# Optimization experiments

Measured on AMD Instinct MI355X. Metric: run time of the kernel, lower is better.

Reference implementation:

```python
import jax, jax.numpy as jnp
import numpy as np

N_ITEMS = 100000
N_USERS = 16384
HIST = 50
TEXT_DIM = 256
GCN_DIM = 128
HIDDEN_DIM = 512
TOWER_DIM = 128


def _l2norm(x, eps=1e-12):
    # F.normalize(dim=1): x / max(||x||, eps)
    n = jnp.sqrt(jnp.sum(x * x, axis=1, keepdims=True))
    return x / jnp.maximum(n, eps)


def setup_inputs() -> dict:
    key = jax.random.key(0)
    ks = jax.random.split(key, 10)
    s1i = 1.0 / np.sqrt(TEXT_DIM + GCN_DIM)
    s2i = 1.0 / np.sqrt(HIDDEN_DIM)
    s1u = 1.0 / np.sqrt(GCN_DIM + TOWER_DIM)
    return {
        "item_text_emb": jax.random.normal(ks[0], (N_ITEMS, TEXT_DIM), jnp.float32),
        "gcn_item_emb": jax.random.normal(ks[1], (N_ITEMS, GCN_DIM), jnp.float32),
        "gcn_user_emb": jax.random.normal(ks[2], (N_USERS, GCN_DIM), jnp.float32),
        "hist_idx": jax.random.randint(ks[3], (N_USERS, HIST), 0, N_ITEMS),
        "W1i": jax.random.normal(ks[4], (TEXT_DIM + GCN_DIM, HIDDEN_DIM), jnp.float32) * s1i,
        "b1i": jnp.zeros((HIDDEN_DIM,), jnp.float32),
        "W2i": jax.random.normal(ks[5], (HIDDEN_DIM, TOWER_DIM), jnp.float32) * s2i,
        "b2i": jnp.zeros((TOWER_DIM,), jnp.float32),
        "W1u": jax.random.normal(ks[6], (GCN_DIM + TOWER_DIM, HIDDEN_DIM), jnp.float32) * s1u,
        "b1u": jnp.zeros((HIDDEN_DIM,), jnp.float32),
        "W2u": jax.random.normal(ks[7], (HIDDEN_DIM, TOWER_DIM), jnp.float32) * s2i,
        "b2u": jnp.zeros((TOWER_DIM,), jnp.float32),
    }


def reference(item_text_emb, gcn_item_emb, gcn_user_emb, hist_idx,
              W1i, b1i, W2i, b2i, W1u, b1u, W2u, b2u):
    # encode_items: MLP over concat(text, gcn) features, then L2 normalize
    item_feat = jnp.concatenate([item_text_emb, gcn_item_emb], axis=1)  # [N_items, text+gcn]
    h = jax.nn.relu(item_feat @ W1i + b1i)
    item_emb = _l2norm(h @ W2i + b2i)  # [N_items, TOWER_DIM]
    # encode_users: per-user gather of history item embeddings + mean pooling
    hist = jnp.mean(item_emb[hist_idx], axis=1)  # [N_users, TOWER_DIM]
    fused = jnp.concatenate([gcn_user_emb, hist], axis=1)
    hu = jax.nn.relu(fused @ W1u + b1u)
    user_emb = _l2norm(hu @ W2u + b2u)  # [N_users, TOWER_DIM]
    return user_emb
```

## Files before the change

### kernel.cpp

```cpp
#include <hip/hip_runtime.h>
#include <hip/hip_bf16.h>

#define HIST 50

typedef __bf16 bf8 __attribute__((ext_vector_type(8)));
typedef float  f4  __attribute__((ext_vector_type(4)));

__device__ __forceinline__ unsigned short f2bf(float x) {
    unsigned u = __builtin_bit_cast(unsigned, x);
    u += 0x7fffu + ((u >> 16) & 1u);
    return (unsigned short)(u >> 16);
}
__device__ __forceinline__ float bf2f(unsigned b) {
    unsigned u = b << 16;
    return __builtin_bit_cast(float, u);
}

__global__ void pack_weights(const float* __restrict__ W1i, const float* __restrict__ W2i,
                             const float* __restrict__ W1u, const float* __restrict__ W2u,
                             unsigned short* __restrict__ dstbase)
{
    int i = blockIdx.x * 256 + threadIdx.x;
    const float* W; unsigned short* dst; int N, KS, loc;
    if (i < 24576)      { W = W1i; dst = dstbase;          N = 512; KS = 12; loc = i; }
    else if (i < 32768) { W = W2i; dst = dstbase + 196608; N = 128; KS = 16; loc = i - 24576; }
    else if (i < 49152) { W = W1u; dst = dstbase + 262144; N = 512; KS = 8;  loc = i - 32768; }
    else                { W = W2u; dst = dstbase + 393216; N = 128; KS = 16; loc = i - 49152; }
    int l = loc & 63, fi = loc >> 6;
    int ks = fi % KS, nt = fi / KS;
    int q = l >> 4, c = l & 15;
    const float* src = W + (size_t)(ks * 32 + q * 8) * N + nt * 16 + c;
    unsigned o[4];
    #pragma unroll
    for (int k = 0; k < 4; ++k) {
        unsigned lo = f2bf(src[(2 * k) * N]);
        unsigned hi = f2bf(src[(2 * k + 1) * N]);
        o[k] = lo | (hi << 16);
    }
    uint4 v; v.x = o[0]; v.y = o[1]; v.z = o[2]; v.w = o[3];
    ((uint4*)dst)[(size_t)(nt * KS + ks) * 64 + l] = v;
}

template<int KS1, int ASTR, bool OUT_BF16>
__device__ __forceinline__ void two_layer(
    const unsigned short* As, unsigned short* Hs,
    const float* b1s, const float* b2s, float* sumsq,
    const bf8* __restrict__ w1f, const bf8* __restrict__ w2f,
    void* __restrict__ outp, int row0, int tid)
{
    const int HSTR = 528;
    const int l = tid & 63, w = tid >> 6;
    const int q = l >> 4, c = l & 15;

    f4 acc1[2][8];
    #pragma unroll
    for (int i = 0; i < 2; ++i)
        #pragma unroll
        for (int j = 0; j < 8; ++j) acc1[i][j] = (f4)0.0f;

    const unsigned short* a0p = As + c * ASTR + q * 8;
    const unsigned short* a1p = As + (16 + c) * ASTR + q * 8;
    for (int ks = 0; ks < KS1; ++ks) {
        bf8 a0 = *(const bf8*)(a0p + ks * 32);
        bf8 a1 = *(const bf8*)(a1p + ks * 32);
        const bf8* wp = w1f + ((size_t)(w * 8) * KS1 + ks) * 64 + l;
        #pragma unroll
        for (int nt = 0; nt < 8; ++nt) {
            bf8 b = wp[(size_t)nt * KS1 * 64];
            acc1[0][nt] = __builtin_amdgcn_mfma_f32_16x16x32_bf16(a0, b, acc1[0][nt], 0, 0, 0);
            acc1[1][nt] = __builtin_amdgcn_mfma_f32_16x16x32_bf16(a1, b, acc1[1][nt], 0, 0, 0);
        }
    }
    #pragma unroll
    for (int nt = 0; nt < 8; ++nt) {
        int col = (w * 8 + nt) * 16 + c;
        float bias = b1s[col];
        #pragma unroll
        for (int rt = 0; rt < 2; ++rt)
            #pragma unroll
            for (int reg = 0; reg < 4; ++reg) {
                float h = fmaxf(acc1[rt][nt][reg] + bias, 0.0f);
                Hs[(rt * 16 + q * 4 + reg) * HSTR + col] = f2bf(h);
            }
    }
    __syncthreads();

    f4 acc2[2][2];
    #pragma unroll
    for (int i = 0; i < 2; ++i)
        #pragma unroll
        for (int j = 0; j < 2; ++j) acc2[i][j] = (f4)0.0f;

    const unsigned short* h0p = Hs + c * HSTR + q * 8;
    const unsigned short* h1p = Hs + (16 + c) * HSTR + q * 8;
    for (int ks = 0; ks < 16; ++ks) {
        bf8 a0 = *(const bf8*)(h0p + ks * 32);
        bf8 a1 = *(const bf8*)(h1p + ks * 32);
        #pragma unroll
        for (int j = 0; j < 2; ++j) {
            bf8 b = w2f[(size_t)((w * 2 + j) * 16 + ks) * 64 + l];
            acc2[0][j] = __builtin_amdgcn_mfma_f32_16x16x32_bf16(a0, b, acc2[0][j], 0, 0, 0);
            acc2[1][j] = __builtin_amdgcn_mfma_f32_16x16x32_bf16(a1, b, acc2[1][j], 0, 0, 0);
        }
    }
    float v[2][2][4];
    #pragma unroll
    for (int rt = 0; rt < 2; ++rt)
        #pragma unroll
        for (int j = 0; j < 2; ++j)
            #pragma unroll
            for (int reg = 0; reg < 4; ++reg)
                v[rt][j][reg] = acc2[rt][j][reg] + b2s[(w * 2 + j) * 16 + c];
    #pragma unroll
    for (int rt = 0; rt < 2; ++rt)
        #pragma unroll
        for (int reg = 0; reg < 4; ++reg) {
            float s = v[rt][0][reg] * v[rt][0][reg] + v[rt][1][reg] * v[rt][1][reg];
            s += __shfl_xor(s, 1); s += __shfl_xor(s, 2);
            s += __shfl_xor(s, 4); s += __shfl_xor(s, 8);
            if (c == 0) atomicAdd(&sumsq[rt * 16 + q * 4 + reg], s);
        }
    __syncthreads();
    #pragma unroll
    for (int rt = 0; rt < 2; ++rt)
        #pragma unroll
        for (int reg = 0; reg < 4; ++reg) {
            int row = rt * 16 + q * 4 + reg;
            float inv = 1.0f / fmaxf(sqrtf(sumsq[row]), 1e-12f);
            #pragma unroll
            for (int j = 0; j < 2; ++j) {
                int col = (w * 2 + j) * 16 + c;
                float o = v[rt][j][reg] * inv;
                if (OUT_BF16)
                    ((unsigned short*)outp)[(size_t)(row0 + row) * 128 + col] = f2bf(o);
                else
                    ((float*)outp)[(size_t)(row0 + row) * 128 + col] = o;
            }
        }
}

__global__ __launch_bounds__(256, 2) void item_kernel(
    const float* __restrict__ text, const float* __restrict__ gcn,
    const bf8* __restrict__ w1f, const float* __restrict__ b1,
    const bf8* __restrict__ w2f, const float* __restrict__ b2,
    unsigned short* __restrict__ item_bf)
{
    __shared__ unsigned short As[32 * 392];
    __shared__ unsigned short Hs[32 * 528];
    __shared__ float b1s[512], b2s[128], sumsq[32];
    const int tid = threadIdx.x;
    const int row0 = blockIdx.x * 32;
    const float4* t4 = (const float4*)text;
    const float4* g4 = (const float4*)gcn;
    #pragma unroll
    for (int j = 0; j < 8; ++j) {
        int idx = tid + j * 256; int r = idx >> 6, c4 = idx & 63;
        float4 x = t4[(size_t)(row0 + r) * 64 + c4];
        ushort4 s; s.x = f2bf(x.x); s.y = f2bf(x.y); s.z = f2bf(x.z); s.w = f2bf(x.w);
        *(ushort4*)(As + r * 392 + c4 * 4) = s;
    }
    #pragma unroll
    for (int j = 0; j < 4; ++j) {
        int idx = tid + j * 256; int r = idx >> 5, c4 = idx & 31;
        float4 x = g4[(size_t)(row0 + r) * 32 + c4];
        ushort4 s; s.x = f2bf(x.x); s.y = f2bf(x.y); s.z = f2bf(x.z); s.w = f2bf(x.w);
        *(ushort4*)(As + r * 392 + 256 + c4 * 4) = s;
    }
    b1s[tid] = b1[tid]; b1s[tid + 256] = b1[tid + 256];
    if (tid < 128) b2s[tid] = b2[tid];
    if (tid < 32)  sumsq[tid] = 0.0f;
    __syncthreads();
    two_layer<12, 392, true>(As, Hs, b1s, b2s, sumsq, w1f, w2f, item_bf, row0, tid);
}

__global__ __launch_bounds__(256, 2) void user_kernel(
    const float* __restrict__ gcnu, const int* __restrict__ hist,
    const unsigned short* __restrict__ item_bf,
    const bf8* __restrict__ w1f, const float* __restrict__ b1,
    const bf8* __restrict__ w2f, const float* __restrict__ b2,
    float* __restrict__ outp)
{
    __shared__ unsigned short As[32 * 272];
    __shared__ unsigned short Hs[32 * 528];
    __shared__ float b1s[512], b2s[128], sumsq[32];
    const int tid = threadIdx.x;
    const int u0 = blockIdx.x * 32;
    const float4* g4 = (const float4*)gcnu;
    #pragma unroll
    for (int j = 0; j < 4; ++j) {
        int idx = tid + j * 256; int r = idx >> 5, c4 = idx & 31;
        float4 x = g4[(size_t)(u0 + r) * 32 + c4];
        ushort4 s; s.x = f2bf(x.x); s.y = f2bf(x.y); s.z = f2bf(x.z); s.w = f2bf(x.w);
        *(ushort4*)(As + r * 272 + c4 * 4) = s;
    }
    {
        const int u = tid >> 3, g = tid & 7;
        float f[16];
        #pragma unroll
        for (int k = 0; k < 16; ++k) f[k] = 0.0f;
        const int* hrow = hist + (size_t)(u0 + u) * HIST;
        #pragma unroll 4
        for (int t = 0; t < HIST; ++t) {
            int id = hrow[t];
            const uint4* p = (const uint4*)(item_bf + (size_t)id * 128 + g * 16);
            uint4 x0 = p[0], x1 = p[1];
            unsigned vs[8] = {x0.x, x0.y, x0.z, x0.w, x1.x, x1.y, x1.z, x1.w};
            #pragma unroll
            for (int k = 0; k < 8; ++k) {
                f[2 * k]     += bf2f(vs[k] & 0xffffu);
                f[2 * k + 1] += bf2f(vs[k] >> 16);
            }
        }
        unsigned o[8];
        #pragma unroll
        for (int k = 0; k < 8; ++k)
            o[k] = (unsigned)f2bf(f[2 * k] * 0.02f) | ((unsigned)f2bf(f[2 * k + 1] * 0.02f) << 16);
        uint4 s0; s0.x = o[0]; s0.y = o[1]; s0.z = o[2]; s0.w = o[3];
        uint4 s1; s1.x = o[4]; s1.y = o[5]; s1.z = o[6]; s1.w = o[7];
        *(uint4*)(As + u * 272 + 128 + g * 16) = s0;
        *(uint4*)(As + u * 272 + 128 + g * 16 + 8) = s1;
    }
    b1s[tid] = b1[tid]; b1s[tid + 256] = b1[tid + 256];
    if (tid < 128) b2s[tid] = b2[tid];
    if (tid < 32)  sumsq[tid] = 0.0f;
    __syncthreads();
    two_layer<8, 272, false>(As, Hs, b1s, b2s, sumsq, w1f, w2f, outp, u0, tid);
}

extern "C" void kernel_launch(void* const* d_in, const int* in_sizes, int n_in,
                              void* d_out, int out_size, void* d_ws, size_t ws_size,
                              hipStream_t stream) {
    const float* text = (const float*)d_in[0];
    const float* gcni = (const float*)d_in[1];
    const float* gcnu = (const float*)d_in[2];
    const int*   hist = (const int*)d_in[3];
    const float* W1i  = (const float*)d_in[4];
    const float* b1i  = (const float*)d_in[5];
    const float* W2i  = (const float*)d_in[6];
    const float* b2i  = (const float*)d_in[7];
    const float* W1u  = (const float*)d_in[8];
    const float* b1u  = (const float*)d_in[9];
    const float* W2u  = (const float*)d_in[10];
    const float* b2u  = (const float*)d_in[11];
    float* out = (float*)d_out;

    unsigned short* itemb = (unsigned short*)d_ws;
    unsigned short* pw = itemb + 12800000;

    pack_weights<<<224, 256, 0, stream>>>(W1i, W2i, W1u, W2u, pw);
    item_kernel<<<100000 / 32, 256, 0, stream>>>(
        text, gcni, (const bf8*)pw, b1i, (const bf8*)(pw + 196608), b2i, itemb);
    user_kernel<<<16384 / 32, 256, 0, stream>>>(
        gcnu, hist, itemb, (const bf8*)(pw + 262144), b1u, (const bf8*)(pw + 393216), b2u, out);
}
```

Measured before the change: 349.4 us.

## Alias input and hidden LDS tiles, raise occupancy, stage history indices in LDS

The input tile and hidden-activation tile now share one LDS buffer, with a barrier added before the hidden layer overwrites the inputs. The hidden stride is reduced, launch bounds go from 2 to 4 blocks per SM to raise occupancy, and the K loops are fully unrolled. In the user kernel, history indices are bulk-loaded into LDS before the gather, and bias loads move ahead of it. Higher occupancy may force register spills given the 64 accumulator floats per thread, and the extra barrier adds some sync cost.

```diff
diff --git a/kernel.cpp b/kernel.cpp
--- a/kernel.cpp
+++ b/kernel.cpp
@@ -43,12 +43,12 @@
 
 template<int KS1, int ASTR, bool OUT_BF16>
 __device__ __forceinline__ void two_layer(
-    const unsigned short* As, unsigned short* Hs,
+    unsigned short* U,
     const float* b1s, const float* b2s, float* sumsq,
     const bf8* __restrict__ w1f, const bf8* __restrict__ w2f,
     void* __restrict__ outp, int row0, int tid)
 {
-    const int HSTR = 528;
+    const int HSTR = 520;
     const int l = tid & 63, w = tid >> 6;
     const int q = l >> 4, c = l & 15;
 
@@ -58,19 +58,22 @@
         #pragma unroll
         for (int j = 0; j < 8; ++j) acc1[i][j] = (f4)0.0f;
 
-    const unsigned short* a0p = As + c * ASTR + q * 8;
-    const unsigned short* a1p = As + (16 + c) * ASTR + q * 8;
+    const unsigned short* a0p = U + c * ASTR + q * 8;
+    const unsigned short* a1p = U + (16 + c) * ASTR + q * 8;
+    const bf8* wp = w1f + (size_t)(w * 8) * KS1 * 64 + l;
+    #pragma unroll
     for (int ks = 0; ks < KS1; ++ks) {
         bf8 a0 = *(const bf8*)(a0p + ks * 32);
         bf8 a1 = *(const bf8*)(a1p + ks * 32);
-        const bf8* wp = w1f + ((size_t)(w * 8) * KS1 + ks) * 64 + l;
         #pragma unroll
         for (int nt = 0; nt < 8; ++nt) {
-            bf8 b = wp[(size_t)nt * KS1 * 64];
+            bf8 b = wp[(size_t)nt * KS1 * 64 + ks * 64];
             acc1[0][nt] = __builtin_amdgcn_mfma_f32_16x16x32_bf16(a0, b, acc1[0][nt], 0, 0, 0);
             acc1[1][nt] = __builtin_amdgcn_mfma_f32_16x16x32_bf16(a1, b, acc1[1][nt], 0, 0, 0);
         }
     }
+    __syncthreads();
+    unsigned short* Hs = U;
     #pragma unroll
     for (int nt = 0; nt < 8; ++nt) {
         int col = (w * 8 + nt) * 16 + c;
@@ -93,6 +96,7 @@
 
     const unsigned short* h0p = Hs + c * HSTR + q * 8;
     const unsigned short* h1p = Hs + (16 + c) * HSTR + q * 8;
+    #pragma unroll
     for (int ks = 0; ks < 16; ++ks) {
         bf8 a0 = *(const bf8*)(h0p + ks * 32);
         bf8 a1 = *(const bf8*)(h1p + ks * 32);
@@ -139,14 +143,13 @@
         }
 }
 
-__global__ __launch_bounds__(256, 2) void item_kernel(
+__global__ __launch_bounds__(256, 4) void item_kernel(
     const float* __restrict__ text, const float* __restrict__ gcn,
     const bf8* __restrict__ w1f, const float* __restrict__ b1,
     const bf8* __restrict__ w2f, const float* __restrict__ b2,
     unsigned short* __restrict__ item_bf)
 {
-    __shared__ unsigned short As[32 * 392];
-    __shared__ unsigned short Hs[32 * 528];
+    __shared__ __align__(16) unsigned short U[32 * 520];
     __shared__ float b1s[512], b2s[128], sumsq[32];
     const int tid = threadIdx.x;
     const int row0 = blockIdx.x * 32;
@@ -157,49 +160,55 @@
         int idx = tid + j * 256; int r = idx >> 6, c4 = idx & 63;
         float4 x = t4[(size_t)(row0 + r) * 64 + c4];
         ushort4 s; s.x = f2bf(x.x); s.y = f2bf(x.y); s.z = f2bf(x.z); s.w = f2bf(x.w);
-        *(ushort4*)(As + r * 392 + c4 * 4) = s;
+        *(ushort4*)(U + r * 392 + c4 * 4) = s;
     }
     #pragma unroll
     for (int j = 0; j < 4; ++j) {
         int idx = tid + j * 256; int r = idx >> 5, c4 = idx & 31;
         float4 x = g4[(size_t)(row0 + r) * 32 + c4];
         ushort4 s; s.x = f2bf(x.x); s.y = f2bf(x.y); s.z = f2bf(x.z); s.w = f2bf(x.w);
-        *(ushort4*)(As + r * 392 + 256 + c4 * 4) = s;
+        *(ushort4*)(U + r * 392 + 256 + c4 * 4) = s;
     }
     b1s[tid] = b1[tid]; b1s[tid + 256] = b1[tid + 256];
     if (tid < 128) b2s[tid] = b2[tid];
     if (tid < 32)  sumsq[tid] = 0.0f;
     __syncthreads();
-    two_layer<12, 392, true>(As, Hs, b1s, b2s, sumsq, w1f, w2f, item_bf, row0, tid);
-}
-
-__global__ __launch_bounds__(256, 2) void user_kernel(
+    two_layer<12, 392, true>(U, b1s, b2s, sumsq, w1f, w2f, item_bf, row0, tid);
+}
+
+__global__ __launch_bounds__(256, 4) void user_kernel(
     const float* __restrict__ gcnu, const int* __restrict__ hist,
     const unsigned short* __restrict__ item_bf,
     const bf8* __restrict__ w1f, const float* __restrict__ b1,
     const bf8* __restrict__ w2f, const float* __restrict__ b2,
     float* __restrict__ outp)
 {
-    __shared__ unsigned short As[32 * 272];
-    __shared__ unsigned short Hs[32 * 528];
+    __shared__ __align__(16) unsigned short U[32 * 520];
     __shared__ float b1s[512], b2s[128], sumsq[32];
     const int tid = threadIdx.x;
     const int u0 = blockIdx.x * 32;
+    int* histL = (int*)(U + 32 * 272);
     const float4* g4 = (const float4*)gcnu;
     #pragma unroll
     for (int j = 0; j < 4; ++j) {
         int idx = tid + j * 256; int r = idx >> 5, c4 = idx & 31;
         float4 x = g4[(size_t)(u0 + r) * 32 + c4];
         ushort4 s; s.x = f2bf(x.x); s.y = f2bf(x.y); s.z = f2bf(x.z); s.w = f2bf(x.w);
-        *(ushort4*)(As + r * 272 + c4 * 4) = s;
-    }
+        *(ushort4*)(U + r * 272 + c4 * 4) = s;
+    }
+    for (int i = tid; i < 32 * HIST; i += 256)
+        histL[i] = hist[(size_t)u0 * HIST + i];
+    b1s[tid] = b1[tid]; b1s[tid + 256] = b1[tid + 256];
+    if (tid < 128) b2s[tid] = b2[tid];
+    if (tid < 32)  sumsq[tid] = 0.0f;
+    __syncthreads();
     {
         const int u = tid >> 3, g = tid & 7;
         float f[16];
         #pragma unroll
         for (int k = 0; k < 16; ++k) f[k] = 0.0f;
-        const int* hrow = hist + (size_t)(u0 + u) * HIST;
-        #pragma unroll 4
+        const int* hrow = histL + u * HIST;
+        #pragma unroll 5
         for (int t = 0; t < HIST; ++t) {
             int id = hrow[t];
             const uint4* p = (const uint4*)(item_bf + (size_t)id * 128 + g * 16);
@@ -217,14 +226,11 @@
             o[k] = (unsigned)f2bf(f[2 * k] * 0.02f) | ((unsigned)f2bf(f[2 * k + 1] * 0.02f) << 16);
         uint4 s0; s0.x = o[0]; s0.y = o[1]; s0.z = o[2]; s0.w = o[3];
         uint4 s1; s1.x = o[4]; s1.y = o[5]; s1.z = o[6]; s1.w = o[7];
-        *(uint4*)(As + u * 272 + 128 + g * 16) = s0;
-        *(uint4*)(As + u * 272 + 128 + g * 16 + 8) = s1;
-    }
-    b1s[tid] = b1[tid]; b1s[tid + 256] = b1[tid + 256];
-    if (tid < 128) b2s[tid] = b2[tid];
-    if (tid < 32)  sumsq[tid] = 0.0f;
-    __syncthreads();
-    two_layer<8, 272, false>(As, Hs, b1s, b2s, sumsq, w1f, w2f, outp, u0, tid);
+        *(uint4*)(U + u * 272 + 128 + g * 16) = s0;
+        *(uint4*)(U + u * 272 + 128 + g * 16 + 8) = s1;
+    }
+    __syncthreads();
+    two_layer<8, 272, false>(U, b1s, b2s, sumsq, w1f, w2f, outp, u0, tid);
 }
 
 extern "C" void kernel_launch(void* const* d_in, const int* in_sizes, int n_in,
```

Result: slower. 366.9 us (+5.0%).

## Double row tile to 64 per block and alias input and hidden LDS buffers

Applied to the files above, without the earlier changes.

Each block now handles 64 rows instead of 32, so every weight fragment fetched from global memory feeds four MFMA row tiles instead of two, halving weight traffic per row. The input and hidden activations now share one LDS buffer, with an extra barrier before the hidden layer overwrites the inputs, which keeps shared memory within budget. The K loops are fully unrolled with all A and B fragments loaded up front, and a tail guard handles the partial last item block. The history gather uses four threads per user instead of eight. The trade-off is higher register pressure from 32 accumulators per thread, which may cut occupancy or cause spills, and fewer blocks to spread across the GPU.

```diff
diff --git a/kernel.cpp b/kernel.cpp
--- a/kernel.cpp
+++ b/kernel.cpp
@@ -2,6 +2,8 @@
 #include <hip/hip_bf16.h>
 
 #define HIST 50
+#define N_ITEMS 100000
+#define N_USERS 16384
 
 typedef __bf16 bf8 __attribute__((ext_vector_type(8)));
 typedef float  f4  __attribute__((ext_vector_type(4)));
@@ -42,77 +44,88 @@
 }
 
 template<int KS1, int ASTR, bool OUT_BF16>
-__device__ __forceinline__ void two_layer(
-    const unsigned short* As, unsigned short* Hs,
-    const float* b1s, const float* b2s, float* sumsq,
+__device__ __forceinline__ void tower_core(
+    unsigned short* U, const float* b1s, const float* b2s, float* sumsq,
     const bf8* __restrict__ w1f, const bf8* __restrict__ w2f,
-    void* __restrict__ outp, int row0, int tid)
-{
-    const int HSTR = 528;
+    void* __restrict__ outp, int row0, int nval, int tid)
+{
+    const int HSTR = 520;
     const int l = tid & 63, w = tid >> 6;
     const int q = l >> 4, c = l & 15;
 
-    f4 acc1[2][8];
-    #pragma unroll
-    for (int i = 0; i < 2; ++i)
+    f4 acc1[4][8];
+    #pragma unroll
+    for (int i = 0; i < 4; ++i)
         #pragma unroll
         for (int j = 0; j < 8; ++j) acc1[i][j] = (f4)0.0f;
 
-    const unsigned short* a0p = As + c * ASTR + q * 8;
-    const unsigned short* a1p = As + (16 + c) * ASTR + q * 8;
+    const unsigned short* ap = U + c * ASTR + q * 8;
+    #pragma unroll
     for (int ks = 0; ks < KS1; ++ks) {
-        bf8 a0 = *(const bf8*)(a0p + ks * 32);
-        bf8 a1 = *(const bf8*)(a1p + ks * 32);
-        const bf8* wp = w1f + ((size_t)(w * 8) * KS1 + ks) * 64 + l;
-        #pragma unroll
-        for (int nt = 0; nt < 8; ++nt) {
-            bf8 b = wp[(size_t)nt * KS1 * 64];
-            acc1[0][nt] = __builtin_amdgcn_mfma_f32_16x16x32_bf16(a0, b, acc1[0][nt], 0, 0, 0);
-            acc1[1][nt] = __builtin_amdgcn_mfma_f32_16x16x32_bf16(a1, b, acc1[1][nt], 0, 0, 0);
-        }
-    }
+        bf8 a[4], b[8];
+        #pragma unroll
+        for (int rt = 0; rt < 4; ++rt)
+            a[rt] = *(const bf8*)(ap + rt * 16 * ASTR + ks * 32);
+        #pragma unroll
+        for (int nt = 0; nt < 8; ++nt)
+            b[nt] = w1f[(size_t)((w * 8 + nt) * KS1 + ks) * 64 + l];
+        #pragma unroll
+        for (int rt = 0; rt < 4; ++rt)
+            #pragma unroll
+            for (int nt = 0; nt < 8; ++nt)
+                acc1[rt][nt] = __builtin_amdgcn_mfma_f32_16x16x32_bf16(a[rt], b[nt], acc1[rt][nt], 0, 0, 0);
+    }
+    __syncthreads();
+
     #pragma unroll
     for (int nt = 0; nt < 8; ++nt) {
-        int col = (w * 8 + nt) * 16 + c;
+        int col = w * 128 + nt * 16 + c;
         float bias = b1s[col];
         #pragma unroll
-        for (int rt = 0; rt < 2; ++rt)
+        for (int rt = 0; rt < 4; ++rt)
             #pragma unroll
             for (int reg = 0; reg < 4; ++reg) {
                 float h = fmaxf(acc1[rt][nt][reg] + bias, 0.0f);
-                Hs[(rt * 16 + q * 4 + reg) * HSTR + col] = f2bf(h);
+                U[(rt * 16 + q * 4 + reg) * HSTR + col] = f2bf(h);
             }
     }
     __syncthreads();
 
-    f4 acc2[2][2];
-    #pragma unroll
-    for (int i = 0; i < 2; ++i)
+    f4 acc2[4][2];
+    #pragma unroll
+    for (int i = 0; i < 4; ++i)
         #pragma unroll
         for (int j = 0; j < 2; ++j) acc2[i][j] = (f4)0.0f;
 
-    const unsigned short* h0p = Hs + c * HSTR + q * 8;
-    const unsigned short* h1p = Hs + (16 + c) * HSTR + q * 8;
+    const unsigned short* hp = U + c * HSTR + q * 8;
+    #pragma unroll
     for (int ks = 0; ks < 16; ++ks) {
-        bf8 a0 = *(const bf8*)(h0p + ks * 32);
-        bf8 a1 = *(const bf8*)(h1p + ks * 32);
+        bf8 a[4], b[2];
+        #pragma unroll
+        for (int rt = 0; rt < 4; ++rt)
+            a[rt] = *(const bf8*)(hp + rt * 16 * HSTR + ks * 32);
+        #pragma unroll
+        for (int j = 0; j < 2; ++j)
+            b[j] = w2f[(size_t)((w * 2 + j) * 16 + ks) * 64 + l];
+        #pragma unroll
+        for (int rt = 0; rt < 4; ++rt)
+            #pragma unroll
+            for (int j = 0; j < 2; ++j)
+                acc2[rt][j] = __builtin_amdgcn_mfma_f32_16x16x32_bf16(a[rt], b[j], acc2[rt][j], 0, 0, 0);
+    }
+
+    float v[4][2][4];
+    #pragma unroll
+    for (int rt = 0; rt < 4; ++rt)
         #pragma unroll
         for (int j = 0; j < 2; ++j) {
-            bf8 b = w2f[(size_t)((w * 2 + j) * 16 + ks) * 64 + l];
-            acc2[0][j] = __builtin_amdgcn_mfma_f32_16x16x32_bf16(a0, b, acc2[0][j], 0, 0, 0);
-            acc2[1][j] = __builtin_amdgcn_mfma_f32_16x16x32_bf16(a1, b, acc2[1][j], 0, 0, 0);
-        }
-    }
-    float v[2][2][4];
-    #pragma unroll
-    for (int rt = 0; rt < 2; ++rt)
-        #pragma unroll
-        for (int j = 0; j < 2; ++j)
+            float bias = b2s[w * 32 + j * 16 + c];
             #pragma unroll
             for (int reg = 0; reg < 4; ++reg)
-                v[rt][j][reg] = acc2[rt][j][reg] + b2s[(w * 2 + j) * 16 + c];
-    #pragma unroll
-    for (int rt = 0; rt < 2; ++rt)
+                v[rt][j][reg] = acc2[rt][j][reg] + bias;
+        }
+    #pragma unroll
+    for (int rt = 0; rt < 4; ++rt)
         #pragma unroll
         for (int reg = 0; reg < 4; ++reg) {
             float s = v[rt][0][reg] * v[rt][0][reg] + v[rt][1][reg] * v[rt][1][reg];
@@ -122,22 +135,27 @@
         }
     __syncthreads();
     #pragma unroll
-    for (int rt = 0; rt < 2; ++rt)
+    for (int rt = 0; rt < 4; ++rt)
         #pragma unroll
         for (int reg = 0; reg < 4; ++reg) {
             int row = rt * 16 + q * 4 + reg;
-            float inv = 1.0f / fmaxf(sqrtf(sumsq[row]), 1e-12f);
-            #pragma unroll
-            for (int j = 0; j < 2; ++j) {
-                int col = (w * 2 + j) * 16 + c;
-                float o = v[rt][j][reg] * inv;
-                if (OUT_BF16)
-                    ((unsigned short*)outp)[(size_t)(row0 + row) * 128 + col] = f2bf(o);
-                else
-                    ((float*)outp)[(size_t)(row0 + row) * 128 + col] = o;
+            if (row < nval) {
+                float inv = 1.0f / fmaxf(sqrtf(sumsq[row]), 1e-12f);
+                #pragma unroll
+                for (int j = 0; j < 2; ++j) {
+                    int col = w * 32 + j * 16 + c;
+                    float o = v[rt][j][reg] * inv;
+                    if (OUT_BF16)
+                        ((unsigned short*)outp)[(size_t)(row0 + row) * 128 + col] = f2bf(o);
+                    else
+                        ((float*)outp)[(size_t)(row0 + row) * 128 + col] = o;
+                }
             }
         }
 }
+
+#define ASI 392
+#define ASU 264
 
 __global__ __launch_bounds__(256, 2) void item_kernel(
     const float* __restrict__ text, const float* __restrict__ gcn,
@@ -145,32 +163,32 @@
     const bf8* __restrict__ w2f, const float* __restrict__ b2,
     unsigned short* __restrict__ item_bf)
 {
-    __shared__ unsigned short As[32 * 392];
-    __shared__ unsigned short Hs[32 * 528];
-    __shared__ float b1s[512], b2s[128], sumsq[32];
+    __shared__ __align__(16) unsigned short U[64 * 520];
+    __shared__ float b1s[512], b2s[128], sumsq[64];
     const int tid = threadIdx.x;
-    const int row0 = blockIdx.x * 32;
+    const int row0 = blockIdx.x * 64;
+    const int nval = min(64, N_ITEMS - row0);
     const float4* t4 = (const float4*)text;
     const float4* g4 = (const float4*)gcn;
     #pragma unroll
+    for (int j = 0; j < 16; ++j) {
+        int idx = tid + j * 256; int r = idx >> 6, c4 = idx & 63;
+        float4 x = (r < nval) ? t4[(size_t)(row0 + r) * 64 + c4] : make_float4(0.f,0.f,0.f,0.f);
+        ushort4 s; s.x = f2bf(x.x); s.y = f2bf(x.y); s.z = f2bf(x.z); s.w = f2bf(x.w);
+        *(ushort4*)(U + r * ASI + c4 * 4) = s;
+    }
+    #pragma unroll
     for (int j = 0; j < 8; ++j) {
-        int idx = tid + j * 256; int r = idx >> 6, c4 = idx & 63;
-        float4 x = t4[(size_t)(row0 + r) * 64 + c4];
+        int idx = tid + j * 256; int r = idx >> 5, c4 = idx & 31;
+        float4 x = (r < nval) ? g4[(size_t)(row0 + r) * 32 + c4] : make_float4(0.f,0.f,0.f,0.f);
         ushort4 s; s.x = f2bf(x.x); s.y = f2bf(x.y); s.z = f2bf(x.z); s.w = f2bf(x.w);
-        *(ushort4*)(As + r * 392 + c4 * 4) = s;
-    }
-    #pragma unroll
-    for (int j = 0; j < 4; ++j) {
-        int idx = tid + j * 256; int r = idx >> 5, c4 = idx & 31;
-        float4 x = g4[(size_t)(row0 + r) * 32 + c4];
-        ushort4 s; s.x = f2bf(x.x); s.y = f2bf(x.y); s.z = f2bf(x.z); s.w = f2bf(x.w);
-        *(ushort4*)(As + r * 392 + 256 + c4 * 4) = s;
+        *(ushort4*)(U + r * ASI + 256 + c4 * 4) = s;
     }
     b1s[tid] = b1[tid]; b1s[tid + 256] = b1[tid + 256];
     if (tid < 128) b2s[tid] = b2[tid];
-    if (tid < 32)  sumsq[tid] = 0.0f;
-    __syncthreads();
-    two_layer<12, 392, true>(As, Hs, b1s, b2s, sumsq, w1f, w2f, item_bf, row0, tid);
+    if (tid < 64)  sumsq[tid] = 0.0f;
+    __syncthreads();
+    tower_core<12, ASI, true>(U, b1s, b2s, sumsq, w1f, w2f, item_bf, row0, nval, tid);
 }
 
 __global__ __launch_bounds__(256, 2) void user_kernel(
@@ -180,51 +198,55 @@
     const bf8* __restrict__ w2f, const float* __restrict__ b2,
     float* __restrict__ outp)
 {
-    __shared__ unsigned short As[32 * 272];
-    __shared__ unsigned short Hs[32 * 528];
-    __shared__ float b1s[512], b2s[128], sumsq[32];
+    __shared__ __align__(16) unsigned short U[64 * 520];
+    __shared__ float b1s[512], b2s[128], sumsq[64];
     const int tid = threadIdx.x;
-    const int u0 = blockIdx.x * 32;
+    const int u0 = blockIdx.x * 64;
     const float4* g4 = (const float4*)gcnu;
     #pragma unroll
-    for (int j = 0; j < 4; ++j) {
+    for (int j = 0; j < 8; ++j) {
         int idx = tid + j * 256; int r = idx >> 5, c4 = idx & 31;
         float4 x = g4[(size_t)(u0 + r) * 32 + c4];
         ushort4 s; s.x = f2bf(x.x); s.y = f2bf(x.y); s.z = f2bf(x.z); s.w = f2bf(x.w);
-        *(ushort4*)(As + r * 272 + c4 * 4) = s;
-    }
+        *(ushort4*)(U + r * ASU + c4 * 4) = s;
+    }
+    b1s[tid] = b1[tid]; b1s[tid + 256] = b1[tid + 256];
+    if (tid < 128) b2s[tid] = b2[tid];
+    if (tid < 64)  sumsq[tid] = 0.0f;
     {
-        const int u = tid >> 3, g = tid & 7;
-        float f[16];
-        #pragma unroll
-        for (int k = 0; k < 16; ++k) f[k] = 0.0f;
+        const int u = tid >> 2, g = tid & 3;
+        float f[32];
+        #pragma unroll
+        for (int k = 0; k < 32; ++k) f[k] = 0.0f;
         const int* hrow = hist + (size_t)(u0 + u) * HIST;
-        #pragma unroll 4
+        #pragma unroll 5
         for (int t = 0; t < HIST; ++t) {
             int id = hrow[t];
-            const uint4* p = (const uint4*)(item_bf + (size_t)id * 128 + g * 16);
-            uint4 x0 = p[0], x1 = p[1];
-            unsigned vs[8] = {x0.x, x0.y, x0.z, x0.w, x1.x, x1.y, x1.z, x1.w};
-            #pragma unroll
-            for (int k = 0; k < 8; ++k) {
-                f[2 * k]     += bf2f(vs[k] & 0xffffu);
-                f[2 * k + 1] += bf2f(vs[k] >> 16);
+            const uint4* p = (const uint4*)(item_bf + (size_t)id * 128 + g * 32);
+            #pragma unroll
+            for (int h = 0; h < 4; ++h) {
+                uint4 x = p[h];
+                unsigned vs[4] = {x.x, x.y, x.z, x.w};
+                #pragma unroll
+                for (int k = 0; k < 4; ++k) {
+                    f[h * 8 + 2 * k]     += bf2f(vs[k] & 0xffffu);
+                    f[h * 8 + 2 * k + 1] += bf2f(vs[k] >> 16);
+                }
             }
         }
-        unsigned o[8];
-        #pragma unroll
-        for (int k = 0; k < 8; ++k)
+        unsigned o[16];
+        #pragma unroll
+        for (int k = 0; k < 16; ++k)
             o[k] = (unsigned)f2bf(f[2 * k] * 0.02f) | ((unsigned)f2bf(f[2 * k + 1] * 0.02f) << 16);
-        uint4 s0; s0.x = o[0]; s0.y = o[1]; s0.z = o[2]; s0.w = o[3];
-        uint4 s1; s1.x = o[4]; s1.y = o[5]; s1.z = o[6]; s1.w = o[7];
-        *(uint4*)(As + u * 272 + 128 + g * 16) = s0;
-        *(uint4*)(As + u * 272 + 128 + g * 16 + 8) = s1;
-    }
-    b1s[tid] = b1[tid]; b1s[tid + 256] = b1[tid + 256];
-    if (tid < 128) b2s[tid] = b2[tid];
-    if (tid < 32)  sumsq[tid] = 0.0f;
-    __syncthreads();
-    two_layer<8, 272, false>(As, Hs, b1s, b2s, sumsq, w1f, w2f, outp, u0, tid);
+        unsigned short* dstp = U + u * ASU + 128 + g * 32;
+        #pragma unroll
+        for (int h = 0; h < 4; ++h) {
+            uint4 s; s.x = o[h*4]; s.y = o[h*4+1]; s.z = o[h*4+2]; s.w = o[h*4+3];
+            *(uint4*)(dstp + h * 8) = s;
+        }
+    }
+    __syncthreads();
+    tower_core<8, ASU, false>(U, b1s, b2s, sumsq, w1f, w2f, outp, u0, 64, tid);
 }
 
 extern "C" void kernel_launch(void* const* d_in, const int* in_sizes, int n_in,
@@ -248,8 +270,8 @@
     unsigned short* pw = itemb + 12800000;
 
     pack_weights<<<224, 256, 0, stream>>>(W1i, W2i, W1u, W2u, pw);
-    item_kernel<<<100000 / 32, 256, 0, stream>>>(
+    item_kernel<<<(N_ITEMS + 63) / 64, 256, 0, stream>>>(
         text, gcni, (const bf8*)pw, b1i, (const bf8*)(pw + 196608), b2i, itemb);
-    user_kernel<<<16384 / 32, 256, 0, stream>>>(
+    user_kernel<<<N_USERS / 64, 256, 0, stream>>>(
         gcnu, hist, itemb, (const bf8*)(pw + 262144), b1u, (const bf8*)(pw + 393216), b2u, out);
 }
```

Result: no change. 342.7 us (-1.9%).
